# Kernel optimization log

Hardware: AMD Instinct MI355X
Metric: run time of the kernel (lower is better)

Reference implementation:

```python
import jax, jax.numpy as jnp
from jax import lax
import numpy as np

DIM = 512
NUM_HEADS = 8
SR = 2


def setup_inputs() -> dict:
    key = jax.random.key(0)
    ks = jax.random.split(key, 7)
    B, H, W = 4, 64, 64
    N = H * W
    C = DIM
    s = 0.02
    return {
        "x": jax.random.normal(ks[0], (B, N, C), dtype=jnp.float32),
        "q_w": jax.random.normal(ks[1], (C, C), dtype=jnp.float32) * s,
        "kv_w": jax.random.normal(ks[2], (2 * C, C), dtype=jnp.float32) * s,
        "sr_w": jax.random.normal(ks[3], (C, C, SR, SR), dtype=jnp.float32) * s,
        "sr_b": jax.random.normal(ks[4], (C,), dtype=jnp.float32) * s,
        "proj_w": jax.random.normal(ks[5], (C, C), dtype=jnp.float32) * s,
        "proj_b": jax.random.normal(ks[6], (C,), dtype=jnp.float32) * s,
        "H": H,
        "W": W,
    }


def reference(x, q_w, kv_w, sr_w, sr_b, proj_w, proj_b, H, W):
    B, N, C = x.shape
    nh = NUM_HEADS
    hd = C // nh
    scale = hd ** -0.5

    # q projection: [B, nh, N, hd]
    q = (x @ q_w.T).reshape(B, N, nh, hd).transpose(0, 2, 1, 3)

    # spatial reduction via strided conv (kernel=stride=SR)
    x_ = x.transpose(0, 2, 1).reshape(B, C, H, W)
    x_ = lax.conv_general_dilated(
        x_, sr_w, window_strides=(SR, SR), padding="VALID",
        dimension_numbers=("NCHW", "OIHW", "NCHW"),
    ) + sr_b[None, :, None, None]
    Nk = (H // SR) * (W // SR)
    x_ = x_.reshape(B, C, Nk).transpose(0, 2, 1)  # [B, Nk, C]

    # kv projection: [2, B, nh, Nk, hd]
    kv = (x_ @ kv_w.T).reshape(B, Nk, 2, nh, hd).transpose(2, 0, 3, 1, 4)
    k, v = kv[0], kv[1]

    attn = jax.nn.softmax(jnp.einsum("bhnd,bhmd->bhnm", q, k) * scale, axis=-1)
    out = jnp.einsum("bhnm,bhmd->bhnd", attn, v)  # [B, nh, N, hd]
    out = out.transpose(0, 2, 1, 3).reshape(B, N, C)
    return out @ proj_w.T + proj_b
```

## Files before the change

### kernel.cpp

```cpp
#include <hip/hip_runtime.h>


typedef __attribute__((ext_vector_type(8)))  short short8;
typedef __attribute__((ext_vector_type(8)))  unsigned short ushort8;
typedef __attribute__((ext_vector_type(4)))  float floatx4;
typedef __attribute__((ext_vector_type(16))) float floatx16;

__device__ inline unsigned short bf16r(float f) {
    union { float f; unsigned u; } v; v.f = f;
    unsigned r = v.u + 0x7fffu + ((v.u >> 16) & 1u);
    return (unsigned short)(r >> 16);
}

__device__ inline unsigned long long pack4ull(float4 v) {
    return (unsigned long long)bf16r(v.x)
         | ((unsigned long long)bf16r(v.y) << 16)
         | ((unsigned long long)bf16r(v.z) << 32)
         | ((unsigned long long)bf16r(v.w) << 48);
}

__device__ inline ushort8 pack8(float4 a, float4 b) {
    ushort8 o;
    o[0] = bf16r(a.x); o[1] = bf16r(a.y); o[2] = bf16r(a.z); o[3] = bf16r(a.w);
    o[4] = bf16r(b.x); o[5] = bf16r(b.y); o[6] = bf16r(b.z); o[7] = bf16r(b.w);
    return o;
}

__device__ inline void gl_lds16(const void* g, void* l) {
    __builtin_amdgcn_global_load_lds(
        (const __attribute__((address_space(1))) unsigned int*)g,
        (__attribute__((address_space(3))) unsigned int*)l, 16, 0, 0);
}

__global__ __launch_bounds__(256)
void prep(const float* __restrict__ x,  const float* __restrict__ qw,
          const float* __restrict__ kvw, const float* __restrict__ srw,
          const float* __restrict__ pw,
          unsigned short* __restrict__ xb,  unsigned short* __restrict__ qwb,
          unsigned short* __restrict__ kvwb, unsigned short* __restrict__ srwb,
          unsigned short* __restrict__ pwb, unsigned short* __restrict__ xrb) {
    const int bid = blockIdx.x;
    if (bid < 2048) {
        const int id = bid * 256 + threadIdx.x;
        const int cq = id & 127, m = id >> 7;
        const int c0 = cq * 4;
        const int b = m >> 10, rem = m & 1023;
        const int oi = rem >> 5, oj = rem & 31;
        const int n00 = oi * 128 + oj * 2;
        const float* bp = x + ((size_t)(b * 4096 + n00)) * 512 + c0;
        const float4 r00 = *(const float4*)bp;
        const float4 r01 = *(const float4*)(bp + 512);
        const float4 r10 = *(const float4*)(bp + 64 * 512);
        const float4 r11 = *(const float4*)(bp + 65 * 512);
        const unsigned long long w00 = pack4ull(r00), w01 = pack4ull(r01),
                                 w10 = pack4ull(r10), w11 = pack4ull(r11);
        unsigned short* xo = xb + ((size_t)(b * 4096 + n00)) * 512 + c0;
        *(unsigned long long*)(xo)            = w00;
        *(unsigned long long*)(xo + 512)      = w01;
        *(unsigned long long*)(xo + 64 * 512) = w10;
        *(unsigned long long*)(xo + 65 * 512) = w11;
        unsigned short* xd = xrb + (size_t)m * 2048 + c0 * 4;
        #pragma unroll
        for (int j = 0; j < 4; ++j) {
            const unsigned long long e =
                  ((w00 >> (16 * j)) & 0xffffull)
                | (((w01 >> (16 * j)) & 0xffffull) << 16)
                | (((w10 >> (16 * j)) & 0xffffull) << 32)
                | (((w11 >> (16 * j)) & 0xffffull) << 48);
            *(unsigned long long*)(xd + j * 4) = e;
        }
    } else {
        const int b2 = bid - 2048;
        const float* src; unsigned short* dst; int off; float sc = 1.f;
        if (b2 < 128)      { src = qw;  dst = qwb;  off = b2 * 256;
                             sc = 0.18033688011112042f;  }
        else if (b2 < 384) { src = kvw; dst = kvwb; off = (b2 - 128) * 256; }
        else if (b2 < 896) { src = srw; dst = srwb; off = (b2 - 384) * 256; }
        else               { src = pw;  dst = pwb;  off = (b2 - 896) * 256; }
        const int idx = off + threadIdx.x;
        float4 a = *(const float4*)(src + (size_t)idx * 8);
        float4 bq = *(const float4*)(src + (size_t)idx * 8 + 4);
        a.x *= sc; a.y *= sc; a.z *= sc; a.w *= sc;
        bq.x *= sc; bq.y *= sc; bq.z *= sc; bq.w *= sc;
        *(ushort8*)(dst + (size_t)idx * 8) = pack8(a, bq);
    }
}

__device__ __forceinline__ void g_stage(
        const unsigned short* __restrict__ A, const unsigned short* __restrict__ B,
        int K, int bm, int bn, int k0, int t,
        unsigned short* AsB, unsigned short* BsB) {
    #pragma unroll
    for (int i = 0; i < 4; ++i) {
        const int c = i * 256 + t;
        const int r = c >> 3, ch = c & 7;
        gl_lds16(A + (size_t)(bm + r) * K + k0 + ((ch ^ (r & 7)) * 8), AsB + c * 8);
    }
    #pragma unroll
    for (int i = 0; i < 2; ++i) {
        const int c = i * 256 + t;
        const int r = c >> 3, ch = c & 7;
        gl_lds16(B + (size_t)(bn + r) * K + k0 + ((ch ^ (r & 7)) * 8), BsB + c * 8);
    }
}

__device__ __forceinline__ void g_comp(
        const unsigned short* AsB, const unsigned short* BsB,
        int lq, int quad, int wrow, floatx4 (&acc)[2][4]) {
    short8 bf[2][4];
    #pragma unroll
    for (int kc = 0; kc < 2; ++kc)
        #pragma unroll
        for (int ni = 0; ni < 4; ++ni) {
            const int r = ni * 16 + lq;
            bf[kc][ni] = *(const short8*)&BsB[r * 64 + (((kc * 4 + quad) ^ (r & 7)) * 8)];
        }
    #pragma unroll
    for (int mi = 0; mi < 2; ++mi) {
        const int r = wrow + mi * 16 + lq;
        #pragma unroll
        for (int kc = 0; kc < 2; ++kc) {
            const short8 af = *(const short8*)&AsB[r * 64 + (((kc * 4 + quad) ^ (r & 7)) * 8)];
            #pragma unroll
            for (int ni = 0; ni < 4; ++ni)
                acc[mi][ni] = __builtin_amdgcn_mfma_f32_16x16x32_bf16(
                    af, bf[kc][ni], acc[mi][ni], 0, 0, 0);
        }
    }
}

__device__ __forceinline__ void g_run(
        const unsigned short* __restrict__ A, const unsigned short* __restrict__ B,
        int K, int bm, int bn, int t, int lq, int quad, int wrow,
        unsigned short (&As)[2][128 * 64], unsigned short (&Bs)[2][64 * 64],
        floatx4 (&acc)[2][4]) {
    g_stage(A, B, K, bm, bn, 0, t, As[0], Bs[0]);
    __syncthreads();
    const int nk = K >> 6;
    for (int ks = 0; ks < nk; ++ks) {
        const int cur = ks & 1;
        if (ks + 1 < nk)
            g_stage(A, B, K, bm, bn, (ks + 1) * 64, t, As[cur ^ 1], Bs[cur ^ 1]);
        __builtin_amdgcn_s_setprio(1);
        g_comp(As[cur], Bs[cur], lq, quad, wrow, acc);
        __builtin_amdgcn_s_setprio(0);
        if (ks + 1 < nk) __syncthreads();
    }
}

__global__ __launch_bounds__(256)
void gemm_qc(const unsigned short* __restrict__ xb, const unsigned short* __restrict__ qwb,
             const unsigned short* __restrict__ xrb, const unsigned short* __restrict__ srwb,
             const float* __restrict__ sr_b,
             unsigned short* __restrict__ qb, unsigned short* __restrict__ xsrb) {
    __shared__ unsigned short As[2][128 * 64];
    __shared__ unsigned short Bs[2][64 * 64];
    const int t = threadIdx.x;
    const int w = t >> 6, l = t & 63;
    const int lq = l & 15, quad = l >> 4;
    const int wrow = w * 32;
    const int bx = blockIdx.x;
    const unsigned short *A, *B; int K, bm; const float* bias; unsigned short* C;
    if (bx < 128) { A = xb;  B = qwb;  K = 512;  bm = bx * 128;         bias = nullptr; C = qb;   }
    else          { A = xrb; B = srwb; K = 2048; bm = (bx - 128) * 128; bias = sr_b;    C = xsrb; }
    const int bn = blockIdx.y * 64;

    floatx4 acc[2][4];
    #pragma unroll
    for (int mi = 0; mi < 2; ++mi)
        #pragma unroll
        for (int ni = 0; ni < 4; ++ni) acc[mi][ni] = (floatx4){0.f, 0.f, 0.f, 0.f};

    g_run(A, B, K, bm, bn, t, lq, quad, wrow, As, Bs, acc);

    #pragma unroll
    for (int ni = 0; ni < 4; ++ni) {
        const int col = bn + ni * 16 + lq;
        const float bv = bias ? bias[col] : 0.f;
        #pragma unroll
        for (int mi = 0; mi < 2; ++mi) {
            const int row0 = bm + wrow + mi * 16 + quad * 4;
            unsigned own[4], mg[4];
            #pragma unroll
            for (int r = 0; r < 4; ++r) own[r] = bf16r(acc[mi][ni][r] + bv);
            #pragma unroll
            for (int r = 0; r < 4; ++r) {
                const unsigned pt = __shfl_xor(own[r], 1);
                mg[r] = (lq & 1) ? (pt | (own[r] << 16)) : (own[r] | (pt << 16));
            }
            const int colb = bn + ni * 16 + (lq & ~1);
            const int rb = (lq & 1) * 2;
            *(unsigned*)(C + (size_t)(row0 + rb)     * 512 + colb) = mg[rb];
            *(unsigned*)(C + (size_t)(row0 + rb + 1) * 512 + colb) = mg[rb + 1];
        }
    }
}

__global__ __launch_bounds__(256)
void gemm_kv(const unsigned short* __restrict__ kvwb, const unsigned short* __restrict__ xsrb,
             unsigned short* __restrict__ Kb, unsigned short* __restrict__ Vt) {
    __shared__ unsigned short As[2][128 * 64];
    __shared__ unsigned short Bs[2][64 * 64];
    const int t = threadIdx.x;
    const int w = t >> 6, l = t & 63;
    const int lq = l & 15, quad = l >> 4;
    const int wrow = w * 32;
    const int id = blockIdx.x;
    const bool isK = id < 256;
    const unsigned short* A = isK ? kvwb : xsrb;
    const unsigned short* B = isK ? xsrb : kvwb + (size_t)512 * 512;
    const int bm = isK ? (id & 3) * 128 : ((id - 256) >> 3) * 128;
    const int bn = isK ? (id >> 2) * 64 : ((id - 256) & 7) * 64;

    floatx4 acc[2][4];
    #pragma unroll
    for (int mi = 0; mi < 2; ++mi)
        #pragma unroll
        for (int ni = 0; ni < 4; ++ni) acc[mi][ni] = (floatx4){0.f, 0.f, 0.f, 0.f};

    g_run(A, B, 512, bm, bn, t, lq, quad, wrow, As, Bs, acc);

    #pragma unroll
    for (int ni = 0; ni < 4; ++ni) {
        const int col = bn + ni * 16 + lq;
        #pragma unroll
        for (int mi = 0; mi < 2; ++mi) {
            const int row0 = bm + wrow + mi * 16 + quad * 4;
            unsigned long long wv = 0;
            #pragma unroll
            for (int r = 0; r < 4; ++r)
                wv |= (unsigned long long)bf16r(acc[mi][ni][r]) << (16 * r);
            if (isK) {
                const int kb = col >> 10, key = col & 1023;
                const int h = row0 >> 6, d0 = row0 & 63;
                *(unsigned long long*)(Kb +
                    (((size_t)(kb * 8 + h)) * 1024 + key) * 64 + d0) = wv;
            } else {
                const int kb = row0 >> 10, key0 = row0 & 1023;
                const int h = col >> 6, d = col & 63;
                *(unsigned long long*)(Vt +
                    (((size_t)(kb * 8 + h)) * 64 + d) * 1024 + key0) = wv;
            }
        }
    }
}

__global__ __launch_bounds__(256)
void gemm_proj(const unsigned short* __restrict__ attb, const unsigned short* __restrict__ pwb,
               const float* __restrict__ pb, float* __restrict__ out) {
    __shared__ unsigned short As[2][128 * 64];
    __shared__ unsigned short Bs[2][64 * 64];
    const int t = threadIdx.x;
    const int w = t >> 6, l = t & 63;
    const int lq = l & 15, quad = l >> 4;
    const int wrow = w * 32;
    const int bm = blockIdx.x * 128, bn = blockIdx.y * 64;

    floatx4 acc[2][4];
    #pragma unroll
    for (int mi = 0; mi < 2; ++mi)
        #pragma unroll
        for (int ni = 0; ni < 4; ++ni) acc[mi][ni] = (floatx4){0.f, 0.f, 0.f, 0.f};

    g_run(attb, pwb, 512, bm, bn, t, lq, quad, wrow, As, Bs, acc);

    #pragma unroll
    for (int ni = 0; ni < 4; ++ni) {
        const int col = bn + ni * 16 + lq;
        const float bv = pb[col];
        #pragma unroll
        for (int mi = 0; mi < 2; ++mi) {
            const int row0 = bm + wrow + mi * 16 + quad * 4;
            #pragma unroll
            for (int r = 0; r < 4; ++r)
                out[(size_t)(row0 + r) * 512 + col] = acc[mi][ni][r] + bv;
        }
    }
}

__global__ __launch_bounds__(256)
void attn_mfma32(const unsigned short* __restrict__ qb,
                 const unsigned short* __restrict__ Kb,
                 const unsigned short* __restrict__ Vt,
                 unsigned short* __restrict__ out) {
    __shared__ unsigned short Ks[2][64 * 64];
    __shared__ unsigned short Vs[2][64 * 64];

    const int t = threadIdx.x;
    const int w = t >> 6;
    const int lane = t & 63;
    const int m32 = lane & 31;
    const int sig = lane >> 5;
    const int n0 = blockIdx.x * 128;
    const int bh = blockIdx.y;
    const int b = bh >> 3, h = bh & 7;

    short8 qf[4];
    {
        const unsigned short* qrow =
            qb + ((size_t)(b * 4096 + n0 + w * 32 + m32)) * 512 + h * 64;
        #pragma unroll
        for (int kc = 0; kc < 4; ++kc)
            qf[kc] = *(const short8*)(qrow + kc * 16 + sig * 8);
    }

    float l_own = 0.f;
    floatx16 O0, O1;
    #pragma unroll
    for (int i = 0; i < 16; ++i) { O0[i] = 0.f; O1[i] = 0.f; }

    const unsigned short* Kg = Kb + (size_t)bh * 1024 * 64;
    const unsigned short* Vg = Vt + (size_t)bh * 64 * 1024;

    #pragma unroll
    for (int i = 0; i < 2; ++i) {
        const int c = i * 256 + t;
        const int r = c >> 3, ch = c & 7;
        const int sw = (ch ^ (r & 7)) * 8;
        gl_lds16(Kg + (size_t)r * 64 + sw, &Ks[0][c * 8]);
        gl_lds16(Vg + (size_t)r * 1024 + sw, &Vs[0][c * 8]);
    }
    __syncthreads();

    for (int kt = 0; kt < 16; ++kt) {
        const int cur = kt & 1;
        if (kt < 15) {
            #pragma unroll
            for (int i = 0; i < 2; ++i) {
                const int c = i * 256 + t;
                const int r = c >> 3, ch = c & 7;
                const int sw = (ch ^ (r & 7)) * 8;
                gl_lds16(Kg + ((size_t)((kt + 1) * 64 + r)) * 64 + sw,
                         &Ks[cur ^ 1][c * 8]);
                gl_lds16(Vg + (size_t)r * 1024 + (kt + 1) * 64 + sw,
                         &Vs[cur ^ 1][c * 8]);
            }
        }
        const unsigned short* KsC = Ks[cur];
        const unsigned short* VsC = Vs[cur];

        floatx16 st0, st1;
        #pragma unroll
        for (int i = 0; i < 16; ++i) { st0[i] = 0.f; st1[i] = 0.f; }
        __builtin_amdgcn_s_setprio(1);
        #pragma unroll
        for (int kc = 0; kc < 4; ++kc) {
            const int swo = (((kc * 2 + sig) ^ (m32 & 7)) * 8);
            const short8 a0 = *(const short8*)&KsC[m32 * 64 + swo];
            st0 = __builtin_amdgcn_mfma_f32_32x32x16_bf16(a0, qf[kc], st0, 0, 0, 0);
            const short8 a1 = *(const short8*)&KsC[(32 + m32) * 64 + swo];
            st1 = __builtin_amdgcn_mfma_f32_32x32x16_bf16(a1, qf[kc], st1, 0, 0, 0);
        }
        __builtin_amdgcn_s_setprio(0);

        uint2 E[2][4];
        #pragma unroll
        for (int g = 0; g < 2; ++g) {
            #pragma unroll
            for (int qd = 0; qd < 4; ++qd) {
                const float p0 = __builtin_amdgcn_exp2f(g ? st1[qd * 4 + 0] : st0[qd * 4 + 0]);
                const float p1 = __builtin_amdgcn_exp2f(g ? st1[qd * 4 + 1] : st0[qd * 4 + 1]);
                const float p2 = __builtin_amdgcn_exp2f(g ? st1[qd * 4 + 2] : st0[qd * 4 + 2]);
                const float p3 = __builtin_amdgcn_exp2f(g ? st1[qd * 4 + 3] : st0[qd * 4 + 3]);
                E[g][qd].x = __builtin_amdgcn_perm(
                    __float_as_uint(p1), __float_as_uint(p0), 0x07060302u);
                E[g][qd].y = __builtin_amdgcn_perm(
                    __float_as_uint(p3), __float_as_uint(p2), 0x07060302u);
                l_own += (p0 + p1) + (p2 + p3);
            }
        }

        #pragma unroll
        for (int kc = 0; kc < 4; ++kc) {
            const int g = kc >> 1, qlo = (kc & 1) * 2;
            unsigned ax = E[g][qlo].x, bx_ = E[g][qlo + 1].x;
            unsigned ay = E[g][qlo].y, by_ = E[g][qlo + 1].y;
            asm("v_permlane32_swap_b32 %0, %1" : "+v"(ax), "+v"(bx_));
            asm("v_permlane32_swap_b32 %0, %1" : "+v"(ay), "+v"(by_));
            uint4 fr; fr.x = ax; fr.y = ay; fr.z = bx_; fr.w = by_;
            const short8 pa = *(const short8*)&fr;
            const int swo = (((kc * 2 + sig) ^ (m32 & 7)) * 8);
            __builtin_amdgcn_s_setprio(1);
            const short8 v0 = *(const short8*)&VsC[m32 * 64 + swo];
            O0 = __builtin_amdgcn_mfma_f32_32x32x16_bf16(pa, v0, O0, 0, 0, 0);
            const short8 v1 = *(const short8*)&VsC[(32 + m32) * 64 + swo];
            O1 = __builtin_amdgcn_mfma_f32_32x32x16_bf16(pa, v1, O1, 0, 0, 0);
            __builtin_amdgcn_s_setprio(0);
        }

        if (kt < 15) __syncthreads();
    }

    l_own += __shfl_xor(l_own, 32);
    const float inv = 1.0f / l_own;

    float fo0[16], fo1[16];
    #pragma unroll
    for (int r = 0; r < 16; ++r) {
        const float li = __shfl(inv, ((r & 3) + 8 * (r >> 2)) + 4 * sig);
        fo0[r] = O0[r] * li;
        fo1[r] = O1[r] * li;
    }

    #pragma unroll
    for (int gd = 0; gd < 2; ++gd) {
        unsigned mg[16];
        #pragma unroll
        for (int r = 0; r < 16; ++r) {
            const unsigned own = bf16r(gd ? fo1[r] : fo0[r]);
            const unsigned pt = __shfl_xor(own, 1);
            mg[r] = (m32 & 1) ? (pt | (own << 16)) : (own | (pt << 16));
        }
        if ((m32 & 1) == gd) {
            const int colb = h * 64 + gd * 32 + (m32 & ~1);
            #pragma unroll
            for (int r = 0; r < 16; ++r) {
                const int qrow = (r & 3) + 8 * (r >> 2) + 4 * sig;
                const size_t row = (size_t)(b * 4096 + n0 + w * 32 + qrow);
                *(unsigned*)(out + row * 512 + colb) = mg[r];
            }
        }
    }
}

extern "C" void kernel_launch(void* const* d_in, const int* in_sizes, int n_in,
                              void* d_out, int out_size, void* d_ws, size_t ws_size,
                              hipStream_t stream) {
    const float* x      = (const float*)d_in[0];
    const float* q_w    = (const float*)d_in[1];
    const float* kv_w   = (const float*)d_in[2];
    const float* sr_w   = (const float*)d_in[3];
    const float* sr_b   = (const float*)d_in[4];
    const float* proj_w = (const float*)d_in[5];
    const float* proj_b = (const float*)d_in[6];
    float* out = (float*)d_out;

    unsigned short* xb   = (unsigned short*)d_ws;
    unsigned short* attb = xb;
    unsigned short* qb   = xb   + (size_t)16384 * 512;
    unsigned short* xrb  = qb   + (size_t)16384 * 512;
    unsigned short* xsrb = xrb  + (size_t)4096 * 2048;
    unsigned short* qwb  = xsrb + (size_t)4096 * 512;
    unsigned short* kvwb = qwb  + (size_t)512 * 512;
    unsigned short* srwb = kvwb + (size_t)1024 * 512;
    unsigned short* pwb  = srwb + (size_t)512 * 2048;
    unsigned short* Kb   = pwb  + (size_t)512 * 512;
    unsigned short* Vt   = Kb   + (size_t)32 * 1024 * 64;

    const dim3 blk(256);

    prep<<<3072, blk, 0, stream>>>(x, q_w, kv_w, sr_w, proj_w,
                                   xb, qwb, kvwb, srwb, pwb, xrb);

    gemm_qc<<<dim3(160, 8), blk, 0, stream>>>(xb, qwb, xrb, srwb, sr_b, qb, xsrb);

    gemm_kv<<<512, blk, 0, stream>>>(kvwb, xsrb, Kb, Vt);

    attn_mfma32<<<dim3(32, 32), blk, 0, stream>>>(qb, Kb, Vt, attb);

    gemm_proj<<<dim3(128, 8), blk, 0, stream>>>(attb, pwb, proj_b, out);
}
```

Baseline: 221.9 us.

## Replace double-buffered async K/V loads with single padded LDS buffer

The attention kernel drops its double-buffered direct global-to-LDS prefetch with XOR swizzle. Each K/V tile is now loaded synchronously through registers into a single LDS buffer padded to a 72-element row stride, with barriers before and after the load. The setprio region is also widened to cover the whole PV MFMA loop. This halves LDS use, which may allow more resident blocks, but global loads no longer overlap compute within a block.

```diff
diff --git a/kernel.cpp b/kernel.cpp
--- a/kernel.cpp
+++ b/kernel.cpp
@@ -278,13 +278,15 @@
     }
 }
 
+#define KS2 72
+
 __global__ __launch_bounds__(256)
 void attn_mfma32(const unsigned short* __restrict__ qb,
                  const unsigned short* __restrict__ Kb,
                  const unsigned short* __restrict__ Vt,
                  unsigned short* __restrict__ out) {
-    __shared__ unsigned short Ks[2][64 * 64];
-    __shared__ unsigned short Vs[2][64 * 64];
+    __shared__ unsigned short Ks[64 * KS2];
+    __shared__ unsigned short Vs[64 * KS2];
 
     const int t = threadIdx.x;
     const int w = t >> 6;
@@ -311,33 +313,22 @@
 
     const unsigned short* Kg = Kb + (size_t)bh * 1024 * 64;
     const unsigned short* Vg = Vt + (size_t)bh * 64 * 1024;
-
-    #pragma unroll
-    for (int i = 0; i < 2; ++i) {
-        const int c = i * 256 + t;
-        const int r = c >> 3, ch = c & 7;
-        const int sw = (ch ^ (r & 7)) * 8;
-        gl_lds16(Kg + (size_t)r * 64 + sw, &Ks[0][c * 8]);
-        gl_lds16(Vg + (size_t)r * 1024 + sw, &Vs[0][c * 8]);
-    }
-    __syncthreads();
+    const int srow = t >> 2;
+    const int sdb  = (t & 3) * 16;
 
     for (int kt = 0; kt < 16; ++kt) {
-        const int cur = kt & 1;
-        if (kt < 15) {
-            #pragma unroll
-            for (int i = 0; i < 2; ++i) {
-                const int c = i * 256 + t;
-                const int r = c >> 3, ch = c & 7;
-                const int sw = (ch ^ (r & 7)) * 8;
-                gl_lds16(Kg + ((size_t)((kt + 1) * 64 + r)) * 64 + sw,
-                         &Ks[cur ^ 1][c * 8]);
-                gl_lds16(Vg + (size_t)r * 1024 + (kt + 1) * 64 + sw,
-                         &Vs[cur ^ 1][c * 8]);
-            }
-        }
-        const unsigned short* KsC = Ks[cur];
-        const unsigned short* VsC = Vs[cur];
+        __syncthreads();
+        {
+            const unsigned short* src = Kg + ((size_t)(kt * 64 + srow)) * 64 + sdb;
+            *(ushort8*)&Ks[srow * KS2 + sdb]     = *(const ushort8*)src;
+            *(ushort8*)&Ks[srow * KS2 + sdb + 8] = *(const ushort8*)(src + 8);
+        }
+        {
+            const unsigned short* src = Vg + (size_t)srow * 1024 + kt * 64 + sdb;
+            *(ushort8*)&Vs[srow * KS2 + sdb]     = *(const ushort8*)src;
+            *(ushort8*)&Vs[srow * KS2 + sdb + 8] = *(const ushort8*)(src + 8);
+        }
+        __syncthreads();
 
         floatx16 st0, st1;
         #pragma unroll
@@ -345,10 +336,9 @@
         __builtin_amdgcn_s_setprio(1);
         #pragma unroll
         for (int kc = 0; kc < 4; ++kc) {
-            const int swo = (((kc * 2 + sig) ^ (m32 & 7)) * 8);
-            const short8 a0 = *(const short8*)&KsC[m32 * 64 + swo];
+            const short8 a0 = *(const short8*)&Ks[m32 * KS2 + kc * 16 + sig * 8];
             st0 = __builtin_amdgcn_mfma_f32_32x32x16_bf16(a0, qf[kc], st0, 0, 0, 0);
-            const short8 a1 = *(const short8*)&KsC[(32 + m32) * 64 + swo];
+            const short8 a1 = *(const short8*)&Ks[(32 + m32) * KS2 + kc * 16 + sig * 8];
             st1 = __builtin_amdgcn_mfma_f32_32x32x16_bf16(a1, qf[kc], st1, 0, 0, 0);
         }
         __builtin_amdgcn_s_setprio(0);
@@ -370,6 +360,7 @@
             }
         }
 
+        __builtin_amdgcn_s_setprio(1);
         #pragma unroll
         for (int kc = 0; kc < 4; ++kc) {
             const int g = kc >> 1, qlo = (kc & 1) * 2;
@@ -379,16 +370,12 @@
             asm("v_permlane32_swap_b32 %0, %1" : "+v"(ay), "+v"(by_));
             uint4 fr; fr.x = ax; fr.y = ay; fr.z = bx_; fr.w = by_;
             const short8 pa = *(const short8*)&fr;
-            const int swo = (((kc * 2 + sig) ^ (m32 & 7)) * 8);
-            __builtin_amdgcn_s_setprio(1);
-            const short8 v0 = *(const short8*)&VsC[m32 * 64 + swo];
+            const short8 v0 = *(const short8*)&Vs[m32 * KS2 + kc * 16 + sig * 8];
             O0 = __builtin_amdgcn_mfma_f32_32x32x16_bf16(pa, v0, O0, 0, 0, 0);
-            const short8 v1 = *(const short8*)&VsC[(32 + m32) * 64 + swo];
+            const short8 v1 = *(const short8*)&Vs[(32 + m32) * KS2 + kc * 16 + sig * 8];
             O1 = __builtin_amdgcn_mfma_f32_32x32x16_bf16(pa, v1, O1, 0, 0, 0);
-            __builtin_amdgcn_s_setprio(0);
-        }
-
-        if (kt < 15) __syncthreads();
+        }
+        __builtin_amdgcn_s_setprio(0);
     }
 
     l_own += __shfl_xor(l_own, 32);
```

Result: no change. 218.8 us (-1.4%).
